# Kernel optimization log

Measured on AMD Instinct MI355X. Metric: run time of the kernel, lower is better.

The kernel has to match this reference:

```python
import jax, jax.numpy as jnp
import numpy as np

DIM = 512
HEADS = 8
DIM_HEAD = 64
SCALE = DIM_HEAD ** -0.5


def setup_inputs() -> dict:
    key = jax.random.key(0)
    ks = jax.random.split(key, 4)
    b, n = 4, 2048
    x = jax.random.normal(ks[0], (b, n, DIM), dtype=jnp.float32)
    Wq = jax.random.normal(ks[1], (DIM, HEADS * DIM_HEAD), dtype=jnp.float32) * (DIM ** -0.5)
    Wkv = jax.random.normal(ks[2], (DIM, 2 * HEADS * DIM_HEAD), dtype=jnp.float32) * (DIM ** -0.5)
    Wo = jax.random.normal(ks[3], (HEADS * DIM_HEAD, DIM), dtype=jnp.float32) * ((HEADS * DIM_HEAD) ** -0.5)
    bo = jnp.zeros((DIM,), dtype=jnp.float32)
    return {"x": x, "Wq": Wq, "Wkv": Wkv, "Wo": Wo, "bo": bo}


def reference(x, Wq, Wkv, Wo, bo):
    b, n, _ = x.shape
    # context = x (self-attention path, kv_include_self=False)
    q = x @ Wq                      # [b, n, h*d]
    kv = x @ Wkv                    # [b, n, 2*h*d]
    k, v = jnp.split(kv, 2, axis=-1)

    def split_heads(t):
        return t.reshape(b, n, HEADS, DIM_HEAD).transpose(0, 2, 1, 3)  # [b,h,n,d]

    q, k, v = split_heads(q), split_heads(k), split_heads(v)
    dots = jnp.einsum('bhid,bhjd->bhij', q, k) * SCALE  # [b,h,n,n]
    attn = jax.nn.softmax(dots, axis=-1)
    out = jnp.einsum('bhij,bhjd->bhid', attn, v)        # [b,h,n,d]
    out = out.transpose(0, 2, 1, 3).reshape(b, n, HEADS * DIM_HEAD)
    return out @ Wo + bo
```

## Files before the change

kernel.cpp:

```cpp
#include <hip/hip_runtime.h>
#include <hip/hip_bf16.h>

typedef short bf16x8 __attribute__((ext_vector_type(8)));
typedef float fx4    __attribute__((ext_vector_type(4)));

#if __has_builtin(__builtin_amdgcn_exp2f)
#define EXP2 __builtin_amdgcn_exp2f
#else
#define EXP2 exp2f
#endif

__device__ __forceinline__ unsigned pk2(float a, float b) {
  union { __hip_bfloat162 h; unsigned u; } cv;
  cv.h = __float22bfloat162_rn(float2{a, b});
  return cv.u;
}
__device__ __forceinline__ uint2 pk4(const fx4& v) {
  uint2 r;
  r.x = pk2(v[0], v[1]);
  r.y = pk2(v[2], v[3]);
  return r;
}

__device__ __forceinline__ void gld16(const void* g, void* l) {
  __builtin_amdgcn_global_load_lds(
      (const __attribute__((address_space(1))) unsigned int*)g,
      (__attribute__((address_space(3))) unsigned int*)l, 16, 0, 0);
}

__global__ __launch_bounds__(256) void cvt_x_kernel(const float* __restrict__ x,
                                                    short* __restrict__ xb, int n4) {
  int i = blockIdx.x * blockDim.x + threadIdx.x;
  if (i < n4) {
    const float4 s = *(const float4*)(x + (size_t)i * 4);
    uint2 o; o.x = pk2(s.x, s.y); o.y = pk2(s.z, s.w);
    *(uint2*)(xb + (size_t)i * 4) = o;
  }
}

__global__ __launch_bounds__(256) void prep_w_kernel(const float* __restrict__ Wq,
                                                     const float* __restrict__ Wkv,
                                                     const float* __restrict__ Wo,
                                                     short* __restrict__ WallT,
                                                     short* __restrict__ WoT,
                                                     float qscale) {
  __shared__ float t[32][33];
  const int bx = blockIdx.x;
  const bool mode0 = bx < 48;
  const int ct = (mode0 ? bx : bx - 48) * 32, kt = blockIdx.y * 32;
  const int tx = threadIdx.x, ty = threadIdx.y;
  short* outT = mode0 ? WallT : WoT;
#pragma unroll
  for (int s = 0; s < 4; ++s) {
    int k = kt + ty + s * 8;
    int c = ct + tx;
    float v;
    if (mode0) v = (c < 512) ? Wq[(size_t)k * 512 + c] * qscale
                             : Wkv[(size_t)k * 1024 + (c - 512)];
    else       v = Wo[(size_t)k * 512 + c];
    t[ty + s * 8][tx] = v;
  }
  __syncthreads();
#pragma unroll
  for (int s = 0; s < 4; ++s) {
    int c = ct + ty + s * 8;
    int k = kt + tx;
    unsigned u = __float_as_uint(t[tx][ty + s * 8]);
    u = (u + 0x7fffu + ((u >> 16) & 1u)) >> 16;
    outT[(size_t)c * 512 + k] = (short)u;
  }
}

__global__ __launch_bounds__(256) void gemm_qkv(
    const short* __restrict__ A, const short* __restrict__ Bt,
    short* __restrict__ oq, short* __restrict__ ok, short* __restrict__ ovT) {
  __shared__ short As[2 * 128 * 32];
  __shared__ short Bs[2 * 128 * 32];
  const int K = 512;
  const int tid = threadIdx.x;
  const int wave = tid >> 6, lane = tid & 63;
  const int quad = lane >> 4, l15 = lane & 15;
  const int wm = wave >> 1, wn = wave & 1;
  const int m0 = blockIdx.y * 128, n0 = blockIdx.x * 128;
  const bool swapped = (n0 < 1024);

  fx4 acc[4][4];
#pragma unroll
  for (int i = 0; i < 4; ++i)
#pragma unroll
    for (int j = 0; j < 4; ++j) acc[i][j] = fx4{0.f, 0.f, 0.f, 0.f};

  for (int k0 = 0; k0 < K; k0 += 64) {
#pragma unroll
    for (int c = 0; c < 4; ++c) {
      int u = c * 256 + tid;
      int slab = u >> 9, r2 = u & 511;
      int row = r2 >> 2, seg = r2 & 3;
      gld16(A  + (size_t)(m0 + row) * K + k0 + slab * 32 + seg * 8,
            As + (size_t)(c * 256 + wave * 64) * 8);
      gld16(Bt + (size_t)(n0 + row) * K + k0 + slab * 32 + seg * 8,
            Bs + (size_t)(c * 256 + wave * 64) * 8);
    }
    __syncthreads();
#pragma unroll
    for (int ks2 = 0; ks2 < 2; ++ks2) {
      bf16x8 af[4], bfr[4];
#pragma unroll
      for (int i = 0; i < 4; ++i)
        af[i] = *(const bf16x8*)(As + ks2 * 4096 + (wm * 64 + i * 16 + l15) * 32 + quad * 8);
#pragma unroll
      for (int i = 0; i < 4; ++i)
        bfr[i] = *(const bf16x8*)(Bs + ks2 * 4096 + (wn * 64 + i * 16 + l15) * 32 + quad * 8);
      if (swapped) {
#pragma unroll
        for (int mi = 0; mi < 4; ++mi)
#pragma unroll
          for (int ni = 0; ni < 4; ++ni)
            acc[mi][ni] = __builtin_amdgcn_mfma_f32_16x16x32_bf16(bfr[ni], af[mi], acc[mi][ni], 0, 0, 0);
      } else {
#pragma unroll
        for (int mi = 0; mi < 4; ++mi)
#pragma unroll
          for (int ni = 0; ni < 4; ++ni)
            acc[mi][ni] = __builtin_amdgcn_mfma_f32_16x16x32_bf16(af[mi], bfr[ni], acc[mi][ni], 0, 0, 0);
      }
    }
    __syncthreads();
  }

  const int rowb = m0 + wm * 64;
  const int colb = n0 + wn * 64;
  const int cls = n0 >> 9;
  if (cls < 2) {
    short* base = (cls == 0) ? oq : ok;
#pragma unroll
    for (int mi = 0; mi < 4; ++mi) {
      int t = rowb + mi * 16 + l15;
      int bb = t >> 11, ii = t & 2047;
#pragma unroll
      for (int ni = 0; ni < 4; ++ni) {
        int f = (colb + ni * 16 + quad * 4) & 511;
        int hh = f >> 6, dd = f & 63;
        *(uint2*)(base + ((size_t)(bb * 8 + hh) * 2048 + ii) * 64 + dd) = pk4(acc[mi][ni]);
      }
    }
  } else {
#pragma unroll
    for (int mi = 0; mi < 4; ++mi) {
      int rbase = rowb + mi * 16 + quad * 4;
      int bb = rbase >> 11;
      int ii = rbase & 2047;
#pragma unroll
      for (int ni = 0; ni < 4; ++ni) {
        int c = (colb + ni * 16 + l15) & 511;
        int hh = c >> 6, dd = c & 63;
        *(uint2*)(ovT + ((size_t)(bb * 8 + hh) * 64 + dd) * 2048 + ii) = pk4(acc[mi][ni]);
      }
    }
  }
}

__global__ __launch_bounds__(256) void gemm_out(
    const short* __restrict__ A, const short* __restrict__ Bt,
    float* __restrict__ of, const float* __restrict__ bias) {
  __shared__ short As[2 * 64 * 32];
  __shared__ short Bs[2 * 128 * 32];
  const int K = 512, N = 512;
  const int tid = threadIdx.x;
  const int wave = tid >> 6, lane = tid & 63;
  const int quad = lane >> 4, l15 = lane & 15;
  const int wm = wave >> 1, wn = wave & 1;
  const int m0 = blockIdx.y * 64, n0 = blockIdx.x * 128;

  fx4 acc[2][4];
#pragma unroll
  for (int i = 0; i < 2; ++i)
#pragma unroll
    for (int j = 0; j < 4; ++j) acc[i][j] = fx4{0.f, 0.f, 0.f, 0.f};

  for (int k0 = 0; k0 < K; k0 += 64) {
#pragma unroll
    for (int c = 0; c < 2; ++c) {
      int u = c * 256 + tid;
      int slab = u >> 8, r2 = u & 255;
      int row = r2 >> 2, seg = r2 & 3;
      gld16(A + (size_t)(m0 + row) * K + k0 + slab * 32 + seg * 8,
            As + (size_t)(c * 256 + wave * 64) * 8);
    }
#pragma unroll
    for (int c = 0; c < 4; ++c) {
      int u = c * 256 + tid;
      int slab = u >> 9, r2 = u & 511;
      int row = r2 >> 2, seg = r2 & 3;
      gld16(Bt + (size_t)(n0 + row) * K + k0 + slab * 32 + seg * 8,
            Bs + (size_t)(c * 256 + wave * 64) * 8);
    }
    __syncthreads();
#pragma unroll
    for (int ks2 = 0; ks2 < 2; ++ks2) {
      bf16x8 af[2], bfr[4];
#pragma unroll
      for (int i = 0; i < 2; ++i)
        af[i] = *(const bf16x8*)(As + ks2 * 2048 + (wm * 32 + i * 16 + l15) * 32 + quad * 8);
#pragma unroll
      for (int i = 0; i < 4; ++i)
        bfr[i] = *(const bf16x8*)(Bs + ks2 * 4096 + (wn * 64 + i * 16 + l15) * 32 + quad * 8);
#pragma unroll
      for (int mi = 0; mi < 2; ++mi)
#pragma unroll
        for (int ni = 0; ni < 4; ++ni)
          acc[mi][ni] = __builtin_amdgcn_mfma_f32_16x16x32_bf16(af[mi], bfr[ni], acc[mi][ni], 0, 0, 0);
    }
    __syncthreads();
  }

  const int rowb = m0 + wm * 32;
  const int colb = n0 + wn * 64;
#pragma unroll
  for (int mi = 0; mi < 2; ++mi)
#pragma unroll
    for (int ni = 0; ni < 4; ++ni) {
      int cg = colb + ni * 16 + l15;
      float bv = bias[cg];
#pragma unroll
      for (int r = 0; r < 4; ++r) {
        int rg = rowb + mi * 16 + quad * 4 + r;
        of[(size_t)rg * N + cg] = acc[mi][ni][r] + bv;
      }
    }
}

__global__ __launch_bounds__(256) void attn_kernel(
    const short* __restrict__ Q, const short* __restrict__ K,
    const short* __restrict__ Vt, short* __restrict__ O) {
  __shared__ short Ks[64 * 64];
  __shared__ short Vs[64 * 64];
  __shared__ short Ps[4 * 16 * 72];

  const int tid = threadIdx.x;
  const int wave = tid >> 6, lane = tid & 63;
  const int quad = lane >> 4, l15 = lane & 15;
  const int bh = blockIdx.y;
  const int b = bh >> 3, h = bh & 7;
  const int i0 = blockIdx.x * 64 + wave * 16;
  short* Pw = Ps + wave * (16 * 72);

  const int idx0 = tid, idx1 = 256 + tid;
  const int row0 = idx0 >> 3, sg0 = (idx0 & 7) ^ (row0 & 7);
  const int row1 = idx1 >> 3, sg1 = (idx1 & 7) ^ (row1 & 7);
  const short* Kb = K + (size_t)bh * 2048 * 64;
  const short* Vb = Vt + (size_t)bh * 64 * 2048;

  bf16x8 qf[2];
#pragma unroll
  for (int ks = 0; ks < 2; ++ks)
    qf[ks] = *(const bf16x8*)(Q + ((size_t)bh * 2048 + i0 + l15) * 64 + ks * 32 + quad * 8);

  bf16x8 ones;
#pragma unroll
  for (int c = 0; c < 8; ++c) ones[c] = (short)0x3F80;

  fx4 oacc[4];
  fx4 acc_l = fx4{0.f, 0.f, 0.f, 0.f};
#pragma unroll
  for (int dt = 0; dt < 4; ++dt) oacc[dt] = fx4{0.f, 0.f, 0.f, 0.f};

  bf16x8 kpre0, kpre1, vpre0, vpre1;
  {
    kpre0 = *(const bf16x8*)(Kb + (size_t)row0 * 64 + sg0 * 8);
    kpre1 = *(const bf16x8*)(Kb + (size_t)row1 * 64 + sg1 * 8);
    vpre0 = *(const bf16x8*)(Vb + (size_t)row0 * 2048 + sg0 * 8);
    vpre1 = *(const bf16x8*)(Vb + (size_t)row1 * 2048 + sg1 * 8);
  }

  for (int j0 = 0; j0 < 2048; j0 += 64) {
    __syncthreads();
    *(bf16x8*)(Ks + idx0 * 8) = kpre0;
    *(bf16x8*)(Ks + idx1 * 8) = kpre1;
    *(bf16x8*)(Vs + idx0 * 8) = vpre0;
    *(bf16x8*)(Vs + idx1 * 8) = vpre1;
    {
      int jn = (j0 + 64) & 2047;
      kpre0 = *(const bf16x8*)(Kb + (size_t)(jn + row0) * 64 + sg0 * 8);
      kpre1 = *(const bf16x8*)(Kb + (size_t)(jn + row1) * 64 + sg1 * 8);
      vpre0 = *(const bf16x8*)(Vb + (size_t)row0 * 2048 + jn + sg0 * 8);
      vpre1 = *(const bf16x8*)(Vb + (size_t)row1 * 2048 + jn + sg1 * 8);
    }
    __syncthreads();

    fx4 s[4];
#pragma unroll
    for (int jt = 0; jt < 4; ++jt) s[jt] = fx4{0.f, 0.f, 0.f, 0.f};
#pragma unroll
    for (int ks = 0; ks < 2; ++ks) {
#pragma unroll
      for (int jt = 0; jt < 4; ++jt) {
        bf16x8 kf = *(const bf16x8*)(Ks + (jt * 16 + l15) * 64 + (((ks * 4 + quad) ^ (l15 & 7)) * 8));
        s[jt] = __builtin_amdgcn_mfma_f32_16x16x32_bf16(kf, qf[ks], s[jt], 0, 0, 0);
      }
    }

#pragma unroll
    for (int jt = 0; jt < 4; ++jt) {
#pragma unroll
      for (int r = 0; r < 4; ++r) s[jt][r] = EXP2(s[jt][r]);
      *(uint2*)(Pw + l15 * 72 + jt * 16 + quad * 4) = pk4(s[jt]);
    }

#pragma unroll
    for (int kj = 0; kj < 2; ++kj) {
      bf16x8 pf = *(const bf16x8*)(Pw + l15 * 72 + kj * 32 + quad * 8);
      acc_l = __builtin_amdgcn_mfma_f32_16x16x32_bf16(ones, pf, acc_l, 0, 0, 0);
#pragma unroll
      for (int dt = 0; dt < 4; ++dt) {
        bf16x8 vf = *(const bf16x8*)(Vs + (dt * 16 + l15) * 64 + (((kj * 4 + quad) ^ (l15 & 7)) * 8));
        oacc[dt] = __builtin_amdgcn_mfma_f32_16x16x32_bf16(vf, pf, oacc[dt], 0, 0, 0);
      }
    }
  }

  float inv = __builtin_amdgcn_rcpf(acc_l[0]);

  size_t rowbase = ((size_t)b * 2048 + i0 + l15) * 512 + h * 64;
#pragma unroll
  for (int dt = 0; dt < 4; ++dt) {
    fx4 o = oacc[dt] * inv;
    *(uint2*)(O + rowbase + dt * 16 + quad * 4) = pk4(o);
  }
}

extern "C" void kernel_launch(void* const* d_in, const int* in_sizes, int n_in,
                              void* d_out, int out_size, void* d_ws, size_t ws_size,
                              hipStream_t stream) {
  const float* x   = (const float*)d_in[0];
  const float* Wq  = (const float*)d_in[1];
  const float* Wkv = (const float*)d_in[2];
  const float* Wo  = (const float*)d_in[3];
  const float* bo  = (const float*)d_in[4];
  float* out = (float*)d_out;

  char* p = (char*)d_ws;
  short* xb    = (short*)p; p += (size_t)8192 * 512 * 2;
  short* WallT = (short*)p; p += (size_t)1536 * 512 * 2;
  short* WoT   = (short*)p; p += (size_t)512 * 512 * 2;
  short* qb    = (short*)p; p += (size_t)32 * 2048 * 64 * 2;
  short* kb    = (short*)p; p += (size_t)32 * 2048 * 64 * 2;
  short* vTb   = (short*)p; p += (size_t)32 * 64 * 2048 * 2;
  short* Ob    = (short*)p; p += (size_t)8192 * 512 * 2;

  const float qscale = 0.125f * 1.4426950408889634f;

  cvt_x_kernel<<<4096, 256, 0, stream>>>(x, xb, 1048576);
  prep_w_kernel<<<dim3(64, 16), dim3(32, 8), 0, stream>>>(Wq, Wkv, Wo, WallT, WoT, qscale);
  gemm_qkv<<<dim3(12, 64), 256, 0, stream>>>(xb, WallT, qb, kb, vTb);
  attn_kernel<<<dim3(32, 32), 256, 0, stream>>>(qb, kb, vTb, Ob);
  gemm_out<<<dim3(4, 128), 256, 0, stream>>>(Ob, WoT, out, bo);
}
```

Baseline: 181.1 us.

## Merge prep kernels and register-prefetch GEMM tiles with raw barriers

Merges the x conversion and weight transpose kernels into a single launch, which removes one kernel launch. Reworks the GEMM main loops so the next K-tile of A (and of B in the output GEMM) is prefetched into registers while the current tile is in LDS. The loops now use one raw s_barrier with explicit waitcnts per iteration instead of two __syncthreads. The attention loop gets the same barrier change. This is meant to hide global-load latency and cut barrier overhead, but it raises register pressure and depends on hand-placed waitcnt counts being correct.

```diff
diff --git a/kernel.cpp b/kernel.cpp
--- a/kernel.cpp
+++ b/kernel.cpp
@@ -28,27 +28,36 @@
       (__attribute__((address_space(3))) unsigned int*)l, 16, 0, 0);
 }
 
-__global__ __launch_bounds__(256) void cvt_x_kernel(const float* __restrict__ x,
-                                                    short* __restrict__ xb, int n4) {
-  int i = blockIdx.x * blockDim.x + threadIdx.x;
-  if (i < n4) {
+__device__ __forceinline__ void bar_raw() {
+  asm volatile("s_barrier" ::: "memory");
+}
+__device__ __forceinline__ void bar_lgkm() {
+  asm volatile("s_waitcnt lgkmcnt(0)\ns_barrier" ::: "memory");
+}
+__device__ __forceinline__ void bar_lgkm_vm4() {
+  asm volatile("s_waitcnt vmcnt(4) lgkmcnt(0)\ns_barrier" ::: "memory");
+}
+__device__ __forceinline__ void cfence() { asm volatile("" ::: "memory"); }
+
+__global__ __launch_bounds__(256) void prep_kernel(
+    const float* __restrict__ x, const float* __restrict__ Wq,
+    const float* __restrict__ Wkv, const float* __restrict__ Wo,
+    short* __restrict__ xb, short* __restrict__ WallT, short* __restrict__ WoT,
+    float qscale) {
+  const int bx = blockIdx.x, tid = threadIdx.x;
+  if (bx < 4096) {
+    int i = bx * 256 + tid;
     const float4 s = *(const float4*)(x + (size_t)i * 4);
     uint2 o; o.x = pk2(s.x, s.y); o.y = pk2(s.z, s.w);
     *(uint2*)(xb + (size_t)i * 4) = o;
-  }
-}
-
-__global__ __launch_bounds__(256) void prep_w_kernel(const float* __restrict__ Wq,
-                                                     const float* __restrict__ Wkv,
-                                                     const float* __restrict__ Wo,
-                                                     short* __restrict__ WallT,
-                                                     short* __restrict__ WoT,
-                                                     float qscale) {
+    return;
+  }
   __shared__ float t[32][33];
-  const int bx = blockIdx.x;
-  const bool mode0 = bx < 48;
-  const int ct = (mode0 ? bx : bx - 48) * 32, kt = blockIdx.y * 32;
-  const int tx = threadIdx.x, ty = threadIdx.y;
+  const int idx = bx - 4096;
+  const int wb = idx & 63, kt = (idx >> 6) * 32;
+  const bool mode0 = wb < 48;
+  const int ct = (mode0 ? wb : wb - 48) * 32;
+  const int tx = tid & 31, ty = tid >> 5;
   short* outT = mode0 ? WallT : WoT;
 #pragma unroll
   for (int s = 0; s < 4; ++s) {
@@ -84,24 +93,47 @@
   const int m0 = blockIdx.y * 128, n0 = blockIdx.x * 128;
   const bool swapped = (n0 < 1024);
 
+  int arow[4], aoff[4];
+#pragma unroll
+  for (int c = 0; c < 4; ++c) {
+    int u = c * 256 + tid;
+    int slab = u >> 9, r2 = u & 511;
+    arow[c] = r2 >> 2;
+    aoff[c] = slab * 32 + (r2 & 3) * 8;
+  }
+
   fx4 acc[4][4];
 #pragma unroll
   for (int i = 0; i < 4; ++i)
 #pragma unroll
     for (int j = 0; j < 4; ++j) acc[i][j] = fx4{0.f, 0.f, 0.f, 0.f};
 
+  bf16x8 apre[4];
+#pragma unroll
+  for (int c = 0; c < 4; ++c)
+    apre[c] = *(const bf16x8*)(A + (size_t)(m0 + arow[c]) * K + aoff[c]);
+
   for (int k0 = 0; k0 < K; k0 += 64) {
+    bar_raw();
+#pragma unroll
+    for (int c = 0; c < 4; ++c)
+      *(bf16x8*)(As + (size_t)(c * 256 + tid) * 8) = apre[c];
 #pragma unroll
     for (int c = 0; c < 4; ++c) {
       int u = c * 256 + tid;
       int slab = u >> 9, r2 = u & 511;
-      int row = r2 >> 2, seg = r2 & 3;
-      gld16(A  + (size_t)(m0 + row) * K + k0 + slab * 32 + seg * 8,
-            As + (size_t)(c * 256 + wave * 64) * 8);
-      gld16(Bt + (size_t)(n0 + row) * K + k0 + slab * 32 + seg * 8,
+      gld16(Bt + (size_t)(n0 + (r2 >> 2)) * K + k0 + slab * 32 + (r2 & 3) * 8,
             Bs + (size_t)(c * 256 + wave * 64) * 8);
     }
-    __syncthreads();
+    cfence();
+    {
+      int kn = (k0 + 64) & 511;
+#pragma unroll
+      for (int c = 0; c < 4; ++c)
+        apre[c] = *(const bf16x8*)(A + (size_t)(m0 + arow[c]) * K + kn + aoff[c]);
+    }
+    bar_lgkm_vm4();
+
 #pragma unroll
     for (int ks2 = 0; ks2 < 2; ++ks2) {
       bf16x8 af[4], bfr[4];
@@ -125,7 +157,6 @@
             acc[mi][ni] = __builtin_amdgcn_mfma_f32_16x16x32_bf16(af[mi], bfr[ni], acc[mi][ni], 0, 0, 0);
       }
     }
-    __syncthreads();
   }
 
   const int rowb = m0 + wm * 64;
@@ -172,30 +203,53 @@
   const int wm = wave >> 1, wn = wave & 1;
   const int m0 = blockIdx.y * 64, n0 = blockIdx.x * 128;
 
+  int arow[2], aoff[2], brow[4], boff[4];
+#pragma unroll
+  for (int c = 0; c < 2; ++c) {
+    int u = c * 256 + tid;
+    int slab = u >> 8, r2 = u & 255;
+    arow[c] = r2 >> 2; aoff[c] = slab * 32 + (r2 & 3) * 8;
+  }
+#pragma unroll
+  for (int c = 0; c < 4; ++c) {
+    int u = c * 256 + tid;
+    int slab = u >> 9, r2 = u & 511;
+    brow[c] = r2 >> 2; boff[c] = slab * 32 + (r2 & 3) * 8;
+  }
+
   fx4 acc[2][4];
 #pragma unroll
   for (int i = 0; i < 2; ++i)
 #pragma unroll
     for (int j = 0; j < 4; ++j) acc[i][j] = fx4{0.f, 0.f, 0.f, 0.f};
 
+  bf16x8 apre[2], bpre[4];
+#pragma unroll
+  for (int c = 0; c < 2; ++c)
+    apre[c] = *(const bf16x8*)(A + (size_t)(m0 + arow[c]) * K + aoff[c]);
+#pragma unroll
+  for (int c = 0; c < 4; ++c)
+    bpre[c] = *(const bf16x8*)(Bt + (size_t)(n0 + brow[c]) * K + boff[c]);
+
   for (int k0 = 0; k0 < K; k0 += 64) {
-#pragma unroll
-    for (int c = 0; c < 2; ++c) {
-      int u = c * 256 + tid;
-      int slab = u >> 8, r2 = u & 255;
-      int row = r2 >> 2, seg = r2 & 3;
-      gld16(A + (size_t)(m0 + row) * K + k0 + slab * 32 + seg * 8,
-            As + (size_t)(c * 256 + wave * 64) * 8);
-    }
-#pragma unroll
-    for (int c = 0; c < 4; ++c) {
-      int u = c * 256 + tid;
-      int slab = u >> 9, r2 = u & 511;
-      int row = r2 >> 2, seg = r2 & 3;
-      gld16(Bt + (size_t)(n0 + row) * K + k0 + slab * 32 + seg * 8,
-            Bs + (size_t)(c * 256 + wave * 64) * 8);
-    }
-    __syncthreads();
+    bar_raw();
+#pragma unroll
+    for (int c = 0; c < 2; ++c)
+      *(bf16x8*)(As + (size_t)(c * 256 + tid) * 8) = apre[c];
+#pragma unroll
+    for (int c = 0; c < 4; ++c)
+      *(bf16x8*)(Bs + (size_t)(c * 256 + tid) * 8) = bpre[c];
+    {
+      int kn = (k0 + 64) & 511;
+#pragma unroll
+      for (int c = 0; c < 2; ++c)
+        apre[c] = *(const bf16x8*)(A + (size_t)(m0 + arow[c]) * K + kn + aoff[c]);
+#pragma unroll
+      for (int c = 0; c < 4; ++c)
+        bpre[c] = *(const bf16x8*)(Bt + (size_t)(n0 + brow[c]) * K + kn + boff[c]);
+    }
+    bar_lgkm();
+
 #pragma unroll
     for (int ks2 = 0; ks2 < 2; ++ks2) {
       bf16x8 af[2], bfr[4];
@@ -211,7 +265,6 @@
         for (int ni = 0; ni < 4; ++ni)
           acc[mi][ni] = __builtin_amdgcn_mfma_f32_16x16x32_bf16(af[mi], bfr[ni], acc[mi][ni], 0, 0, 0);
     }
-    __syncthreads();
   }
 
   const int rowb = m0 + wm * 32;
@@ -266,19 +319,18 @@
   for (int dt = 0; dt < 4; ++dt) oacc[dt] = fx4{0.f, 0.f, 0.f, 0.f};
 
   bf16x8 kpre0, kpre1, vpre0, vpre1;
-  {
-    kpre0 = *(const bf16x8*)(Kb + (size_t)row0 * 64 + sg0 * 8);
-    kpre1 = *(const bf16x8*)(Kb + (size_t)row1 * 64 + sg1 * 8);
-    vpre0 = *(const bf16x8*)(Vb + (size_t)row0 * 2048 + sg0 * 8);
-    vpre1 = *(const bf16x8*)(Vb + (size_t)row1 * 2048 + sg1 * 8);
-  }
+  kpre0 = *(const bf16x8*)(Kb + (size_t)row0 * 64 + sg0 * 8);
+  kpre1 = *(const bf16x8*)(Kb + (size_t)row1 * 64 + sg1 * 8);
+  vpre0 = *(const bf16x8*)(Vb + (size_t)row0 * 2048 + sg0 * 8);
+  vpre1 = *(const bf16x8*)(Vb + (size_t)row1 * 2048 + sg1 * 8);
 
   for (int j0 = 0; j0 < 2048; j0 += 64) {
-    __syncthreads();
+    bar_raw();
     *(bf16x8*)(Ks + idx0 * 8) = kpre0;
     *(bf16x8*)(Ks + idx1 * 8) = kpre1;
     *(bf16x8*)(Vs + idx0 * 8) = vpre0;
     *(bf16x8*)(Vs + idx1 * 8) = vpre1;
+    cfence();
     {
       int jn = (j0 + 64) & 2047;
       kpre0 = *(const bf16x8*)(Kb + (size_t)(jn + row0) * 64 + sg0 * 8);
@@ -286,7 +338,7 @@
       vpre0 = *(const bf16x8*)(Vb + (size_t)row0 * 2048 + jn + sg0 * 8);
       vpre1 = *(const bf16x8*)(Vb + (size_t)row1 * 2048 + jn + sg1 * 8);
     }
-    __syncthreads();
+    bar_lgkm();
 
     fx4 s[4];
 #pragma unroll
@@ -320,7 +372,6 @@
   }
 
   float inv = __builtin_amdgcn_rcpf(acc_l[0]);
-
   size_t rowbase = ((size_t)b * 2048 + i0 + l15) * 512 + h * 64;
 #pragma unroll
   for (int dt = 0; dt < 4; ++dt) {
@@ -350,8 +401,7 @@
 
   const float qscale = 0.125f * 1.4426950408889634f;
 
-  cvt_x_kernel<<<4096, 256, 0, stream>>>(x, xb, 1048576);
-  prep_w_kernel<<<dim3(64, 16), dim3(32, 8), 0, stream>>>(Wq, Wkv, Wo, WallT, WoT, qscale);
+  prep_kernel<<<5120, 256, 0, stream>>>(x, Wq, Wkv, Wo, xb, WallT, WoT, qscale);
   gemm_qkv<<<dim3(12, 64), 256, 0, stream>>>(xb, WallT, qb, kb, vTb);
   attn_kernel<<<dim3(32, 32), 256, 0, stream>>>(qb, kb, vTb, Ob);
   gemm_out<<<dim3(4, 128), 256, 0, stream>>>(Ob, WoT, out, bo);
```

After: 175.9 us. 1.03x faster.
